# Kernel tuning notes

Hardware: AMD Instinct MI355X
Metric: run time of the kernel (lower is better)

The kernel has to match this reference:

```python
import jax, jax.numpy as jnp
import numpy as np

P = 0.9  # CLOP swap probability (init kwarg)


def _index_permute(key, n_element, dim):
    """Faithful port of CLOPLayer._index_permute: sequential conditional
    neighbor swaps over a flat index array, expressed as a lax.scan.
    Swap choices r in {0..4} with probs (1-p/2, p/8, p/8, p/8, p/8);
    r maps to offset {0, +1, -1, +dim, -dim}; swap only if r!=0 and
    0 < idx < n_element (strict >0, matching the original code)."""
    probs = jnp.array([1.0 - P / 2, P / 8, P / 8, P / 8, P / 8], dtype=jnp.float32)
    # loop runs i over abs(range(-n+1, n)) -> 2n-1 steps
    iters = jnp.abs(jnp.arange(-n_element + 1, n_element, dtype=jnp.int32))
    rs = jax.random.choice(key, 5, shape=(iters.shape[0],), p=probs)
    offsets = jnp.array([0, 1, -1, dim, -dim], dtype=jnp.int32)

    def step(perm, inp):
        i, r = inp
        idx = i + offsets[r]
        do = (r != 0) & (idx > 0) & (idx < n_element)
        idx_c = jnp.clip(idx, 0, n_element - 1)
        a = perm[i]
        b = perm[idx_c]
        # conditional swap; when do is False both writes restore originals
        perm = perm.at[i].set(jnp.where(do, b, a))
        perm = perm.at[idx_c].set(jnp.where(do, a, b))
        return perm, None

    perm0 = jnp.arange(n_element, dtype=jnp.int32)
    perm, _ = jax.lax.scan(step, perm0, (iters, rs))
    return perm


def setup_inputs() -> dict:
    key = jax.random.key(0)
    x = jax.random.normal(key, (512, 9, 84, 84), dtype=jnp.float32)
    return {"x": x}


def reference(x):
    B, C, H, W = x.shape
    n = H * W  # n_element of x[0,0]; dim = int(sqrt(n)) == H for square images
    perm = _index_permute(jax.random.key(42), n, H)
    flat = x.reshape(B, C, n)
    # torch.gather(flat, 2, idx) with idx broadcast over (B, C)
    res = jnp.take(flat, perm, axis=2)
    return res.reshape(x.shape)
```

## Files before the change

### kernel.cpp

```cpp
#include <hip/hip_runtime.h>

#define N_ELEM   7056
#define DIM      84
#define M_STEPS  14111
#define N_ROWS   4608
#define NCHUNK   384
#define KSTEPS   37
#define WINW     208
#define TPB      256
#define NJV      1764

#define TRACE_BLOCKS 28
#define GROUPS   16
#define CPG      (NCHUNK / GROUPS)

#define GTPB     512
#define ROWS_PB  2
#define GK       4

__device__ __forceinline__ void threefry2x32(unsigned k0, unsigned k1,
                                             unsigned x0, unsigned x1,
                                             unsigned &o0, unsigned &o1) {
  const unsigned ks0 = k0, ks1 = k1, ks2 = k0 ^ k1 ^ 0x1BD11BDAu;
  x0 += ks0; x1 += ks1;
#define ROTL(x, r) (((x) << (r)) | ((x) >> (32 - (r))))
#define RND(r) { x0 += x1; x1 = ROTL(x1, r); x1 ^= x0; }
  RND(13) RND(15) RND(26) RND(6)
  x0 += ks1; x1 += ks2 + 1u;
  RND(17) RND(29) RND(16) RND(24)
  x0 += ks2; x1 += ks0 + 2u;
  RND(13) RND(15) RND(26) RND(6)
  x0 += ks0; x1 += ks1 + 3u;
  RND(17) RND(29) RND(16) RND(24)
  x0 += ks1; x1 += ks2 + 4u;
  RND(13) RND(15) RND(26) RND(6)
  x0 += ks2; x1 += ks0 + 5u;
  o0 = x0; o1 = x1;
#undef RND
#undef ROTL
}

__device__ __forceinline__ int r_from_bits(unsigned bits) {
  const float p8 = 0.1125f;
  const float q0 = 0.55f;
  const float q1 = q0 + p8;
  const float q2 = q1 + p8;
  const float q3 = q2 + p8;
  const float q4 = q3 + p8;
  float u  = __uint_as_float((bits >> 9) | 0x3F800000u) - 1.0f;
  float rv = q4 * (1.0f - u);
  return (int)(q0 < rv) + (int)(q1 < rv) + (int)(q2 < rv) + (int)(q3 < rv);
}

__device__ __forceinline__ void chunk_bounds(int c, int &t0, int &t1, int &lo, int &hi) {
  t0 = c * KSTEPS; if (t0 > M_STEPS) t0 = M_STEPS;
  t1 = t0 + KSTEPS; if (t1 > M_STEPS) t1 = M_STEPS;
  int a0 = t0 - (N_ELEM - 1);       if (a0 < 0) a0 = -a0;
  int a1 = (t1 - 1) - (N_ELEM - 1); if (a1 < 0) a1 = -a1;
  int imax = a0 > a1 ? a0 : a1;
  int imin;
  if (t0 <= N_ELEM - 1 && t1 - 1 >= N_ELEM - 1) imin = 0;
  else imin = a0 < a1 ? a0 : a1;
  lo = imin - DIM; if (lo < 0) lo = 0;
  hi = imax + DIM; if (hi > N_ELEM - 1) hi = N_ELEM - 1;
}

__global__ __launch_bounds__(TPB) void permbuild_kernel(unsigned short* __restrict__ Pg) {
  __shared__ __align__(16) unsigned short w[CPG * WINW];
  __shared__ unsigned char rs[CPG * KSTEPS];
  const int tid = threadIdx.x;
  const int g  = blockIdx.x / TRACE_BLOCKS;
  const int sb = blockIdx.x % TRACE_BLOCKS;

  for (int idx = tid; idx < CPG * WINW; idx += TPB) {
    int c = idx / WINW;
    int j = idx - c * WINW;
    int t0, t1, lo, hi; chunk_bounds(g * CPG + c, t0, t1, lo, hi);
    w[idx] = (unsigned short)(lo + j);
  }
  for (int q = tid; q < CPG * KSTEPS; q += TPB) {
    int c = q / KSTEPS;
    int k = q - c * KSTEPS;
    int t = (g * CPG + c) * KSTEPS + k;
    unsigned y0, y1;
    threefry2x32(0u, 42u, 0u, (unsigned)t, y0, y1);
    rs[q] = (unsigned char)r_from_bits(y0 ^ y1);
  }
  __syncthreads();

  if (tid < CPG) {
    const int c = tid;
    int t0, t1, lo, hi; chunk_bounds(g * CPG + c, t0, t1, lo, hi);
    const int nt = t1 - t0;
    unsigned short* wc = &w[c * WINW];
    const unsigned char* rc = &rs[c * KSTEPS];
    for (int k = 0; k < nt; ++k) {
      int t = t0 + k;
      int i = t - (N_ELEM - 1); if (i < 0) i = -i;
      int r = rc[k];
      int off = (r == 1) ? 1 : (r == 2) ? -1 : (r == 3) ? DIM : (r == 4) ? -DIM : 0;
      int idx = i + off;
      bool doit = (r != 0) && (idx > 0) && (idx < N_ELEM);
      int je = doit ? idx : i;
      unsigned short a = wc[i  - lo];
      unsigned short b = wc[je - lo];
      wc[i  - lo] = b;
      wc[je - lo] = a;
    }
  }
  __syncthreads();

  if (tid < 252) {
    int y = sb * 252 + tid;
    for (int c = CPG - 1; c >= 0; --c) {
      int t0, t1, lo, hi; chunk_bounds(g * CPG + c, t0, t1, lo, hi);
      unsigned e = (unsigned)(y - lo);
      if (e <= (unsigned)(hi - lo)) y = (int)w[c * WINW + e];
    }
    Pg[g * N_ELEM + sb * 252 + tid] = (unsigned short)y;
  }
}

__global__ __launch_bounds__(TPB) void compose_kernel(const unsigned short* __restrict__ Pg,
                                                      int* __restrict__ permG) {
  const int tid = threadIdx.x;
  if (tid >= 252) return;
  const int j = blockIdx.x * 252 + tid;
  int y = j;
#pragma unroll
  for (int g = GROUPS - 1; g >= 0; --g) y = (int)Pg[g * N_ELEM + y];
  permG[j] = y;
}

__global__ __launch_bounds__(GTPB, 4) void gather_kernel(const float* __restrict__ x,
                                                         const int* __restrict__ perm,
                                                         float* __restrict__ out) {
  __shared__ __align__(16) float row[N_ELEM];
  const int tid = threadIdx.x;
  const int r0 = blockIdx.x * ROWS_PB;
  float4* row4 = (float4*)row;

  int4 p[GK];
  const int4* p4 = (const int4*)perm;
#pragma unroll
  for (int k = 0; k < GK; ++k) {
    int v = tid + k * GTPB;
    if (v < NJV) p[k] = p4[v];
  }

  for (int rr = 0; rr < ROWS_PB; ++rr) {
    const int r = r0 + rr;
    const float4* xr4 = (const float4*)(x + (size_t)r * N_ELEM);
#pragma unroll
    for (int k = 0; k < GK; ++k) {
      int v = tid + k * GTPB;
      if (v < NJV) row4[v] = xr4[v];
    }
    __syncthreads();

    float4* or4 = (float4*)(out + (size_t)r * N_ELEM);
#pragma unroll
    for (int k = 0; k < GK; ++k) {
      int v = tid + k * GTPB;
      if (v < NJV) {
        int4 pp = p[k];
        float4 o;
        o.x = row[pp.x]; o.y = row[pp.y]; o.z = row[pp.z]; o.w = row[pp.w];
        or4[v] = o;
      }
    }
    __syncthreads();
  }
}

extern "C" void kernel_launch(void* const* d_in, const int* in_sizes, int n_in,
                              void* d_out, int out_size, void* d_ws, size_t ws_size,
                              hipStream_t stream) {
  const float* x = (const float*)d_in[0];
  float* out = (float*)d_out;

  unsigned short* Pg = (unsigned short*)d_ws;
  int* perm = (int*)((char*)d_ws + (size_t)GROUPS * N_ELEM * 2);

  permbuild_kernel<<<GROUPS * TRACE_BLOCKS, TPB, 0, stream>>>(Pg);
  compose_kernel<<<TRACE_BLOCKS, TPB, 0, stream>>>(Pg, perm);
  gather_kernel<<<N_ROWS / ROWS_PB, GTPB, 0, stream>>>(x, perm, out);
}
```

Before: 249.8 us.

## Double-buffer gather rows in LDS using async global_load_lds across nine rows

The gather kernel now processes nine rows per block using two LDS row buffers. It stages the next row with direct global-to-LDS loads (`global_load_lds`) while the current row is permuted and written out. This is meant to overlap HBM reads with the LDS gather and store, and to cut register round-trips and block-launch overhead. The trade-off is doubled LDS use per block, which lowers occupancy, and a smaller grid of 512 blocks.

```diff
diff --git a/kernel.cpp b/kernel.cpp
--- a/kernel.cpp
+++ b/kernel.cpp
@@ -15,7 +15,7 @@
 #define CPG      (NCHUNK / GROUPS)
 
 #define GTPB     512
-#define ROWS_PB  2
+#define GROWS    9
 #define GK       4
 
 __device__ __forceinline__ void threefry2x32(unsigned k0, unsigned k1,
@@ -135,10 +135,23 @@
 __global__ __launch_bounds__(GTPB, 4) void gather_kernel(const float* __restrict__ x,
                                                          const int* __restrict__ perm,
                                                          float* __restrict__ out) {
-  __shared__ __align__(16) float row[N_ELEM];
+  __shared__ __align__(16) float rowbuf[2][N_ELEM];
   const int tid = threadIdx.x;
-  const int r0 = blockIdx.x * ROWS_PB;
-  float4* row4 = (float4*)row;
+  const int r0 = blockIdx.x * GROWS;
+
+#define STAGE(dstbuf, gsrc) do {                                               \
+    const float* _g = (gsrc);                                                  \
+    float* _l = (dstbuf);                                                      \
+    _Pragma("unroll")                                                          \
+    for (int _k = 0; _k < GK; ++_k) {                                          \
+      int _v = tid + _k * GTPB;                                                \
+      if (_v < NJV)                                                            \
+        __builtin_amdgcn_global_load_lds(                                      \
+            (const __attribute__((address_space(1))) void*)(_g + _v * 4),      \
+            (__attribute__((address_space(3))) void*)(_l + _v * 4),            \
+            16, 0, 0);                                                         \
+    }                                                                          \
+  } while (0)
 
   int4 p[GK];
   const int4* p4 = (const int4*)perm;
@@ -148,17 +161,16 @@
     if (v < NJV) p[k] = p4[v];
   }
 
-  for (int rr = 0; rr < ROWS_PB; ++rr) {
-    const int r = r0 + rr;
-    const float4* xr4 = (const float4*)(x + (size_t)r * N_ELEM);
-#pragma unroll
-    for (int k = 0; k < GK; ++k) {
-      int v = tid + k * GTPB;
-      if (v < NJV) row4[v] = xr4[v];
-    }
-    __syncthreads();
-
-    float4* or4 = (float4*)(out + (size_t)r * N_ELEM);
+  STAGE(rowbuf[0], x + (size_t)r0 * N_ELEM);
+  __syncthreads();
+
+  int cur = 0;
+  for (int rr = 0; rr < GROWS; ++rr) {
+    if (rr + 1 < GROWS)
+      STAGE(rowbuf[1 - cur], x + (size_t)(r0 + rr + 1) * N_ELEM);
+
+    const float* row = rowbuf[cur];
+    float4* or4 = (float4*)(out + (size_t)(r0 + rr) * N_ELEM);
 #pragma unroll
     for (int k = 0; k < GK; ++k) {
       int v = tid + k * GTPB;
@@ -170,7 +182,9 @@
       }
     }
     __syncthreads();
-  }
+    cur ^= 1;
+  }
+#undef STAGE
 }
 
 extern "C" void kernel_launch(void* const* d_in, const int* in_sizes, int n_in,
@@ -184,5 +198,5 @@
 
   permbuild_kernel<<<GROUPS * TRACE_BLOCKS, TPB, 0, stream>>>(Pg);
   compose_kernel<<<TRACE_BLOCKS, TPB, 0, stream>>>(Pg, perm);
-  gather_kernel<<<N_ROWS / ROWS_PB, GTPB, 0, stream>>>(x, perm, out);
-}
+  gather_kernel<<<N_ROWS / GROWS, GTPB, 0, stream>>>(x, perm, out);
+}
```

After: 252.6 us. Within noise of the previous version (+1.1%).

## Gather with single-wave blocks loading rows directly into LDS

Applied to the files above, without the earlier changes.

The gather kernel now runs one 64-lane wavefront per block and handles four rows per block. Each row is staged into shared memory with `global_load_lds` 16-byte direct-to-LDS loads, so the data no longer passes through registers. The trailing barrier is dropped, relying on single-wave ordering. Each lane now keeps 28 int4 permutation entries in registers. The cost is far fewer resident waves per CU, since each 64-thread block still needs about 28KB of LDS, which may weaken latency hiding.

```diff
diff --git a/kernel.cpp b/kernel.cpp
--- a/kernel.cpp
+++ b/kernel.cpp
@@ -14,9 +14,9 @@
 #define GROUPS   16
 #define CPG      (NCHUNK / GROUPS)
 
-#define GTPB     512
-#define ROWS_PB  2
-#define GK       4
+#define GW       64
+#define GR       4
+#define GKW      28
 
 __device__ __forceinline__ void threefry2x32(unsigned k0, unsigned k1,
                                              unsigned x0, unsigned x1,
@@ -132,36 +132,39 @@
   permG[j] = y;
 }
 
-__global__ __launch_bounds__(GTPB, 4) void gather_kernel(const float* __restrict__ x,
-                                                         const int* __restrict__ perm,
-                                                         float* __restrict__ out) {
+__global__ __launch_bounds__(GW, 1) void gather_kernel(const float* __restrict__ x,
+                                                       const int* __restrict__ perm,
+                                                       float* __restrict__ out) {
   __shared__ __align__(16) float row[N_ELEM];
-  const int tid = threadIdx.x;
-  const int r0 = blockIdx.x * ROWS_PB;
-  float4* row4 = (float4*)row;
+  const int lane = threadIdx.x;
+  const int r0 = blockIdx.x * GR;
 
-  int4 p[GK];
+  int4 p[GKW];
   const int4* p4 = (const int4*)perm;
 #pragma unroll
-  for (int k = 0; k < GK; ++k) {
-    int v = tid + k * GTPB;
+  for (int k = 0; k < GKW; ++k) {
+    int v = lane + k * GW;
     if (v < NJV) p[k] = p4[v];
   }
 
-  for (int rr = 0; rr < ROWS_PB; ++rr) {
-    const int r = r0 + rr;
-    const float4* xr4 = (const float4*)(x + (size_t)r * N_ELEM);
+  for (int rr = 0; rr < GR; ++rr) {
+    const float* xr = x + (size_t)(r0 + rr) * N_ELEM;
+    __builtin_amdgcn_sched_barrier(0);
 #pragma unroll
-    for (int k = 0; k < GK; ++k) {
-      int v = tid + k * GTPB;
-      if (v < NJV) row4[v] = xr4[v];
+    for (int k = 0; k < GKW; ++k) {
+      int v = lane + k * GW;
+      if (v < NJV)
+        __builtin_amdgcn_global_load_lds(
+            (const __attribute__((address_space(1))) void*)(xr + v * 4),
+            (__attribute__((address_space(3))) void*)(row + v * 4),
+            16, 0, 0);
     }
     __syncthreads();
 
-    float4* or4 = (float4*)(out + (size_t)r * N_ELEM);
+    float4* or4 = (float4*)(out + (size_t)(r0 + rr) * N_ELEM);
 #pragma unroll
-    for (int k = 0; k < GK; ++k) {
-      int v = tid + k * GTPB;
+    for (int k = 0; k < GKW; ++k) {
+      int v = lane + k * GW;
       if (v < NJV) {
         int4 pp = p[k];
         float4 o;
@@ -169,7 +172,6 @@
         or4[v] = o;
       }
     }
-    __syncthreads();
   }
 }
 
@@ -184,5 +186,5 @@
 
   permbuild_kernel<<<GROUPS * TRACE_BLOCKS, TPB, 0, stream>>>(Pg);
   compose_kernel<<<TRACE_BLOCKS, TPB, 0, stream>>>(Pg, perm);
-  gather_kernel<<<N_ROWS / ROWS_PB, GTPB, 0, stream>>>(x, perm, out);
+  gather_kernel<<<N_ROWS / GR, GW, 0, stream>>>(x, perm, out);
 }
```

Measured after the change: 256.9 us. 2.8% more time.
